# Kernel optimization log

Measured on AMD Instinct MI355X. Metric: run time of the kernel, lower is better.

## Reference

```python
import jax, jax.numpy as jnp
import numpy as np

NEG_SLOPE = 0.2  # PyG GATConv default negative_slope


def _gat_conv(h, src, dst, N, W, a_src, a_dst, b, heads):
    """PyG GATConv (eval mode, self-loops already in src/dst).
    h: [N, F_in], W: [F_in, heads*C], a_src/a_dst: [heads, C], b: [heads*C]."""
    C = W.shape[1] // heads
    hl = (h @ W).reshape(N, heads, C)                      # [N,H,C]
    al_s = jnp.einsum('nhc,hc->nh', hl, a_src)             # [N,H]
    al_d = jnp.einsum('nhc,hc->nh', hl, a_dst)             # [N,H]
    e = jax.nn.leaky_relu(al_s[src] + al_d[dst], NEG_SLOPE)  # [E,H]
    # segment softmax over incoming edges of each destination node
    m = jax.ops.segment_max(e, dst, num_segments=N)        # [N,H]
    ex = jnp.exp(e - m[dst])
    s = jax.ops.segment_sum(ex, dst, num_segments=N)
    alpha = ex / (s[dst] + 1e-16)                          # [E,H]
    out = jax.ops.segment_sum(hl[src] * alpha[:, :, None], dst, num_segments=N)
    return out.reshape(N, heads * C) + b


def setup_inputs() -> dict:
    key = jax.random.key(0)
    ks = jax.random.split(key, 16)
    N, E, D = 30000, 240000, 64
    NUM_ENT, NUM_REL, NUM_DRUGS = 100000, 64, 200
    sc = 0.1
    return {
        'x': jax.random.randint(ks[0], (N,), 0, NUM_ENT),
        'edge_index': jax.random.randint(ks[1], (2, E), 0, N),
        'edge_type': jax.random.randint(ks[2], (N,), 0, NUM_REL),
        'ent_emb': jax.random.normal(ks[3], (NUM_ENT, D), jnp.float32) * sc,
        'rel_emb': jax.random.normal(ks[4], (NUM_REL, D), jnp.float32) * sc,
        'W1': jax.random.normal(ks[5], (2 * D, 8 * D), jnp.float32) * sc,
        'att1_src': jax.random.normal(ks[6], (8, D), jnp.float32) * sc,
        'att1_dst': jax.random.normal(ks[7], (8, D), jnp.float32) * sc,
        'b1': jax.random.normal(ks[8], (8 * D,), jnp.float32) * sc,
        'W2': jax.random.normal(ks[9], (9 * D, D), jnp.float32) * sc,
        'att2_src': jax.random.normal(ks[10], (1, D), jnp.float32) * sc,
        'att2_dst': jax.random.normal(ks[11], (1, D), jnp.float32) * sc,
        'b2': jax.random.normal(ks[12], (D,), jnp.float32) * sc,
        'fc_w': jax.random.normal(ks[13], (D, NUM_DRUGS), jnp.float32) * sc,
        'fc_b': jax.random.normal(ks[14], (NUM_DRUGS,), jnp.float32) * sc,
    }


def reference(x, edge_index, edge_type, ent_emb, rel_emb, W1, att1_src, att1_dst, b1,
              W2, att2_src, att2_dst, b2, fc_w, fc_b):
    N = x.shape[0]
    loop = jnp.arange(N)
    src = jnp.concatenate([edge_index[0], loop])  # GATConv add_self_loops=True
    dst = jnp.concatenate([edge_index[1], loop])
    ent = ent_emb[x]                               # [N,D]
    rel = rel_emb[edge_type]                       # [N,D]
    h = jnp.concatenate([ent, rel], axis=-1)       # [N,2D]  (dropout is identity in eval)
    h = jax.nn.elu(_gat_conv(h, src, dst, N, W1, att1_src, att1_dst, b1, heads=8))  # [N,8D]
    h = jnp.concatenate([h, ent], axis=-1)         # [N,9D]
    h = jax.nn.elu(_gat_conv(h, src, dst, N, W2, att2_src, att2_dst, b2, heads=1))  # [N,D]
    g = jnp.mean(h, axis=0, keepdims=True)         # [1,D]
    return g @ fc_w + fc_b                         # [1,num_drugs]
```

## Files before the change

### kernel.cpp

```cpp
#include <hip/hip_runtime.h>
#include <math.h>

#define NEG_SLOPE 0.2f

typedef __attribute__((ext_vector_type(8))) short short8;
typedef __attribute__((ext_vector_type(4))) float f32x4;
typedef __attribute__((ext_vector_type(2))) float f32x2;

__device__ __forceinline__ float lrelu(float v) { return v > 0.f ? v : NEG_SLOPE * v; }
__device__ __forceinline__ float elu(float v) { return v > 0.f ? v : (__expf(v) - 1.f); }
__device__ __forceinline__ unsigned short f2b(float f) {
    unsigned u = __float_as_uint(f);
    return (unsigned short)((u + 0x7FFFu + ((u >> 16) & 1u)) >> 16);
}
__device__ __forceinline__ float blo(unsigned v) { return __uint_as_float(v << 16); }
__device__ __forceinline__ float bhi(unsigned v) { return __uint_as_float(v & 0xFFFF0000u); }
__device__ __forceinline__ unsigned packb(float a, float b) {
    return ((unsigned)f2b(b) << 16) | (unsigned)f2b(a);
}
__device__ __forceinline__ unsigned short pack8(float a, float b) {
    return (unsigned short)(__builtin_amdgcn_cvt_pk_fp8_f32(a, b, 0, false) & 0xFFFF);
}
__device__ __forceinline__ f32x2 unpack8(unsigned v) {
    return __builtin_amdgcn_cvt_pk_f32_fp8((int)v, false);
}
__device__ __forceinline__ f32x2 unpack8hi(unsigned v) {
    return __builtin_amdgcn_cvt_pk_f32_fp8((int)v, true);
}
__device__ __forceinline__ unsigned bpack_trunc(f32x2 f) {
    return (__float_as_uint(f.y) & 0xFFFF0000u) | (__float_as_uint(f.x) >> 16);
}
__device__ __forceinline__ int sw(int r, int o) { return (o ^ (r & 7)) << 3; }

__global__ __launch_bounds__(256) void init_k(int* __restrict__ zbase, int zwords,
                                              const float* __restrict__ W1,
                                              const float* __restrict__ W2,
                                              const float* __restrict__ a1s,
                                              const float* __restrict__ a1d,
                                              unsigned short* __restrict__ wsb,
                                              unsigned short* __restrict__ W1t,
                                              unsigned short* __restrict__ W2t) {
    int t = blockIdx.x * blockDim.x + threadIdx.x;
    int stride = gridDim.x * blockDim.x;
    for (int i = t; i < zwords; i += stride) zbase[i] = 0;
    for (int i = t; i < 2048; i += stride) {
        int hh = i >> 7, k = i & 127, h = hh & 7;
        const float* aw = (hh < 8) ? a1s : a1d;
        const float* wr = W1 + (size_t)k * 512 + h * 64;
        float s_ = 0.f;
#pragma unroll 16
        for (int c = 0; c < 64; c++) s_ += wr[c] * aw[h * 64 + c];
        wsb[i] = f2b(s_);
    }
    for (int i = t; i < 512 * 128; i += stride) {
        int n = i >> 7, kk = i & 127;
        W1t[i] = f2b(W1[(size_t)kk * 512 + n]);
    }
    for (int i = t; i < 64 * 576; i += stride) {
        int n = i / 576, k = i % 576;
        W2t[i] = f2b(W2[(size_t)k * 64 + n]);
    }
}

__global__ void prep_k(const int* __restrict__ x, const int* __restrict__ et,
                       const int* __restrict__ ei,
                       const float* __restrict__ ent_emb, const float* __restrict__ rel_emb,
                       unsigned* __restrict__ h1b2, unsigned short* __restrict__ h1q,
                       int* __restrict__ deg, int N, int E) {
    int t = blockIdx.x * blockDim.x + threadIdx.x;
    if (t < N * 64) {
        int n = t >> 6, j = t & 63;
        float v0, v1;
        if (j < 32) {
            const float* e = ent_emb + (size_t)x[n] * 64 + 2 * j;
            v0 = e[0]; v1 = e[1];
        } else {
            const float* r = rel_emb + (size_t)et[n] * 64 + 2 * (j - 32);
            v0 = r[0]; v1 = r[1];
        }
        h1b2[t] = packb(v0, v1);
        h1q[t] = pack8(v0, v1);
    }
    if (t < E + N) {
        int dst = t < E ? ei[E + t] : t - E;
        atomicAdd(&deg[dst], 1);
    }
}

__global__ __launch_bounds__(256) void attn1_k(const unsigned short* __restrict__ A,
                                               const unsigned short* __restrict__ Bt,
                                               float* __restrict__ als, float* __restrict__ ald,
                                               int M) {
    __shared__ __align__(16) unsigned short As[128 * 128];
    __shared__ __align__(16) unsigned short Bs[16 * 128];
    int tid = threadIdx.x;
    int m0 = blockIdx.x * 128;
    for (int c = tid; c < 2048; c += 256) {
        int r = c >> 4, o = c & 15;
        int gr = m0 + r;
        uint4 v = make_uint4(0u, 0u, 0u, 0u);
        if (gr < M) v = *(const uint4*)(A + (size_t)gr * 128 + o * 8);
        *(uint4*)(As + r * 128 + sw(r, o)) = v;
    }
    if (tid < 256) {
        int r = tid >> 4, o = tid & 15;
        uint4 v = *(const uint4*)(Bt + (size_t)r * 128 + o * 8);
        *(uint4*)(Bs + r * 128 + sw(r, o)) = v;
    }
    __syncthreads();
    int w = tid >> 6, lane = tid & 63;
    int wr = w * 32;
    int m16 = lane & 15, quad = lane >> 4;
    f32x4 acc[2] = {};
#pragma unroll
    for (int kk = 0; kk < 128; kk += 32) {
        int ob = (kk >> 3) + quad;
        short8 b = *(const short8*)(Bs + m16 * 128 + sw(m16, ob));
#pragma unroll
        for (int i = 0; i < 2; i++) {
            int r = wr + i * 16 + m16;
            short8 a = *(const short8*)(As + r * 128 + sw(r, ob));
            acc[i] = __builtin_amdgcn_mfma_f32_16x16x32_bf16(a, b, acc[i], 0, 0, 0);
        }
    }
#pragma unroll
    for (int i = 0; i < 2; i++)
#pragma unroll
        for (int reg = 0; reg < 4; reg++) {
            int row = m0 + wr + i * 16 + quad * 4 + reg;
            if (row < M) {
                if (m16 < 8) als[row * 8 + m16] = acc[i][reg];
                else         ald[row * 8 + (m16 - 8)] = acc[i][reg];
            }
        }
}

__global__ __launch_bounds__(256) void scan_k(const int* __restrict__ deg,
                                              int* __restrict__ offs,
                                              int* __restrict__ bstate,
                                              int N, int Etot, int NB) {
    __shared__ int s[256];
    __shared__ int sbase;
    int b = blockIdx.x, t = threadIdx.x;
    int i = b * 256 + t;
    int v = (i < N) ? deg[i] : 0;
    s[t] = v;
    __syncthreads();
    for (int off = 1; off < 256; off <<= 1) {
        int tmp = (t >= off) ? s[t - off] : 0;
        __syncthreads();
        s[t] += tmp;
        __syncthreads();
    }
    int total = s[255];
    if (t == 0) {
        if (b == 0) {
            atomicExch(&bstate[0], (total << 2) | 2);
            sbase = 0;
        } else {
            atomicExch(&bstate[b], (total << 2) | 1);
            int run = 0;
            for (int p = b - 1; p >= 0;) {
                int stv;
                do { stv = atomicAdd(&bstate[p], 0); } while ((stv & 3) == 0);
                run += (stv >> 2);
                if ((stv & 3) == 2) break;
                p--;
            }
            atomicExch(&bstate[b], ((run + total) << 2) | 2);
            sbase = run;
        }
    }
    __syncthreads();
    if (i < N) offs[i] = sbase + s[t] - v;
    if (b == NB - 1 && t == 0) offs[N] = Etot;
}

__global__ void fill_k(const int* __restrict__ ei, int E, int N,
                       const int* __restrict__ offs, int* __restrict__ cursor,
                       int* __restrict__ csr) {
    int e = blockIdx.x * blockDim.x + threadIdx.x;
    if (e >= E + N) return;
    int src = e < E ? ei[e] : e - E;
    int dst = e < E ? ei[E + e] : e - E;
    int pos = offs[dst] + atomicAdd(&cursor[dst], 1);
    csr[pos] = src;
}

__global__ __launch_bounds__(256) void aggG_k(const unsigned short* __restrict__ h1q,
                                              const unsigned* __restrict__ h1b2,
                                              const float* __restrict__ als1,
                                              const float* __restrict__ ald1,
                                              const int* __restrict__ offs,
                                              const int* __restrict__ csr,
                                              unsigned short* __restrict__ Gq,
                                              unsigned* __restrict__ h2u, int N) {
    int wv = threadIdx.x >> 6;
    int t = threadIdx.x & 63;
    int n = blockIdx.x * 4 + wv;
    if (n >= N) return;
    int hh = t & 7;
    float dl = ald1[n * 8 + hh];
    int p0 = offs[n], p1 = offs[n + 1];
    float a0[8] = {}, a1[8] = {};
    float ssacc = 0.f;
    int p = p0;
    for (; p + 1 < p1; p += 2) {
        int sA = csr[p], sB = csr[p + 1];
        float lA = als1[sA * 8 + hh];
        float lB = als1[sB * 8 + hh];
        unsigned hA = h1q[(size_t)sA * 64 + t];
        unsigned hB = h1q[(size_t)sB * 64 + t];
        float xA = __expf(lrelu(lA + dl));
        float xB = __expf(lrelu(lB + dl));
        ssacc += xA + xB;
        f32x2 fA = unpack8(hA);
        f32x2 fB = unpack8(hB);
        float evA[8], evB[8];
#pragma unroll
        for (int h = 0; h < 8; h++) { evA[h] = __shfl(xA, h, 64); evB[h] = __shfl(xB, h, 64); }
#pragma unroll
        for (int h = 0; h < 8; h++) {
            a0[h] += evA[h] * fA.x + evB[h] * fB.x;
            a1[h] += evA[h] * fA.y + evB[h] * fB.y;
        }
    }
    if (p < p1) {
        int sA = csr[p];
        float xA = __expf(lrelu(als1[sA * 8 + hh] + dl));
        ssacc += xA;
        f32x2 fA = unpack8(h1q[(size_t)sA * 64 + t]);
        float evA[8];
#pragma unroll
        for (int h = 0; h < 8; h++) evA[h] = __shfl(xA, h, 64);
#pragma unroll
        for (int h = 0; h < 8; h++) { a0[h] += evA[h] * fA.x; a1[h] += evA[h] * fA.y; }
    }
#pragma unroll
    for (int h = 0; h < 8; h++) {
        float iv = 8.f / (__shfl(ssacc, h, 64) + 1e-16f);
        Gq[(size_t)(n * 8 + h) * 64 + t] = pack8(a0[h] * iv, a1[h] * iv);
    }
    if (t < 32)
        h2u[(size_t)n * 288 + 256 + t] = h1b2[(size_t)n * 64 + t];
}

__global__ __launch_bounds__(256) void gemmG_k(const unsigned char* __restrict__ Gq8,
                                               const unsigned short* __restrict__ W1t,
                                               const float* __restrict__ b1,
                                               unsigned short* __restrict__ h2, int M) {
    __shared__ __align__(16) unsigned short As[128 * 128];
    __shared__ __align__(16) unsigned short Bs[64 * 128];
    int tid = threadIdx.x;
    int m0 = blockIdx.x * 128, h = blockIdx.y;
    for (int c = tid; c < 1024; c += 256) {
        int r = c >> 3, o = c & 7;
        int gr = m0 + r;
        uint4 v = make_uint4(0u, 0u, 0u, 0u);
        if (gr < M) v = *(const uint4*)(Gq8 + ((size_t)gr * 8 + h) * 128 + o * 16);
        uint4 w0, w1;
        w0.x = bpack_trunc(unpack8(v.x));   w0.y = bpack_trunc(unpack8hi(v.x));
        w0.z = bpack_trunc(unpack8(v.y));   w0.w = bpack_trunc(unpack8hi(v.y));
        w1.x = bpack_trunc(unpack8(v.z));   w1.y = bpack_trunc(unpack8hi(v.z));
        w1.z = bpack_trunc(unpack8(v.w));   w1.w = bpack_trunc(unpack8hi(v.w));
        *(uint4*)(As + r * 128 + sw(r, 2 * o)) = w0;
        *(uint4*)(As + r * 128 + sw(r, 2 * o + 1)) = w1;
    }
    for (int c = tid; c < 1024; c += 256) {
        int r = c >> 4, o = c & 15;
        uint4 v = *(const uint4*)(W1t + (size_t)(h * 64 + r) * 128 + o * 8);
        *(uint4*)(Bs + r * 128 + sw(r, o)) = v;
    }
    __syncthreads();
    int w = tid >> 6, lane = tid & 63;
    int wr = w * 32;
    int m16 = lane & 15, quad = lane >> 4;
    f32x4 acc[2][4] = {};
#pragma unroll
    for (int kk = 0; kk < 128; kk += 32) {
        int ob = (kk >> 3) + quad;
        short8 b[4];
#pragma unroll
        for (int j = 0; j < 4; j++) {
            int r = j * 16 + m16;
            b[j] = *(const short8*)(Bs + r * 128 + sw(r, ob));
        }
#pragma unroll
        for (int i = 0; i < 2; i++) {
            int r = wr + i * 16 + m16;
            short8 a = *(const short8*)(As + r * 128 + sw(r, ob));
#pragma unroll
            for (int j = 0; j < 4; j++)
                acc[i][j] = __builtin_amdgcn_mfma_f32_16x16x32_bf16(a, b[j], acc[i][j], 0, 0, 0);
        }
    }
#pragma unroll
    for (int i = 0; i < 2; i++)
#pragma unroll
        for (int j = 0; j < 4; j++)
#pragma unroll
            for (int reg = 0; reg < 4; reg++) {
                int row = m0 + wr + i * 16 + quad * 4 + reg;
                int col = h * 64 + j * 16 + m16;
                if (row < M)
                    h2[(size_t)row * 576 + col] = f2b(elu(acc[i][j][reg] * 0.125f + b1[col]));
            }
}

__global__ __launch_bounds__(256) void gemm2_k(const unsigned short* __restrict__ A,
                                               const unsigned short* __restrict__ Bt,
                                               const float* __restrict__ a2s,
                                               const float* __restrict__ a2d,
                                               unsigned char* __restrict__ hl2q,
                                               float* __restrict__ als2,
                                               float* __restrict__ ald2, int M) {
    __shared__ __align__(16) unsigned short As[64 * 64];
    __shared__ __align__(16) unsigned short Bs[64 * 64];
    int tid = threadIdx.x;
    int m0 = blockIdx.x * 64;
    int w = tid >> 6, lane = tid & 63;
    int m16 = lane & 15, quad = lane >> 4;
    f32x4 acc[4] = {};
    for (int k0 = 0; k0 < 576; k0 += 64) {
        __syncthreads();
        for (int c = tid; c < 512; c += 256) {
            int r = c >> 3, o = c & 7;
            int gr = m0 + r;
            uint4 v = make_uint4(0u, 0u, 0u, 0u);
            if (gr < M) v = *(const uint4*)(A + (size_t)gr * 576 + k0 + o * 8);
            *(uint4*)(As + r * 64 + sw(r, o)) = v;
        }
        for (int c = tid; c < 512; c += 256) {
            int r = c >> 3, o = c & 7;
            uint4 v = *(const uint4*)(Bt + (size_t)r * 576 + k0 + o * 8);
            *(uint4*)(Bs + r * 64 + sw(r, o)) = v;
        }
        __syncthreads();
#pragma unroll
        for (int kk = 0; kk < 64; kk += 32) {
            int ob = (kk >> 3) + quad;
            int r = w * 16 + m16;
            short8 a = *(const short8*)(As + r * 64 + sw(r, ob));
#pragma unroll
            for (int j = 0; j < 4; j++) {
                int rb = j * 16 + m16;
                short8 b = *(const short8*)(Bs + rb * 64 + sw(rb, ob));
                acc[j] = __builtin_amdgcn_mfma_f32_16x16x32_bf16(a, b, acc[j], 0, 0, 0);
            }
        }
    }
#pragma unroll
    for (int j = 0; j < 4; j++)
#pragma unroll
        for (int reg = 0; reg < 4; reg++) {
            int row = m0 + w * 16 + quad * 4 + reg;
            int col = j * 16 + m16;
            if (row < M)
                hl2q[(size_t)row * 64 + col] =
                    (unsigned char)(__builtin_amdgcn_cvt_pk_fp8_f32(acc[j][reg], 0.f, 0, false) & 0xFF);
        }
    float sa[4] = {}, sd[4] = {};
#pragma unroll
    for (int j = 0; j < 4; j++) {
        int col = j * 16 + m16;
        float as_ = a2s[col], ad_ = a2d[col];
#pragma unroll
        for (int reg = 0; reg < 4; reg++) {
            sa[reg] += acc[j][reg] * as_;
            sd[reg] += acc[j][reg] * ad_;
        }
    }
#pragma unroll
    for (int m = 1; m < 16; m <<= 1)
#pragma unroll
        for (int reg = 0; reg < 4; reg++) {
            sa[reg] += __shfl_xor(sa[reg], m, 64);
            sd[reg] += __shfl_xor(sd[reg], m, 64);
        }
    if (m16 == 0)
#pragma unroll
        for (int reg = 0; reg < 4; reg++) {
            int row = m0 + w * 16 + quad * 4 + reg;
            if (row < M) { als2[row] = sa[reg]; ald2[row] = sd[reg]; }
        }
}

__global__ __launch_bounds__(256) void agg2_k(const unsigned short* __restrict__ hl2q16,
                                              const float* __restrict__ als2,
                                              const float* __restrict__ ald2,
                                              const float* __restrict__ b2,
                                              const int* __restrict__ offs,
                                              const int* __restrict__ csr,
                                              float* __restrict__ gpart, int N) {
    __shared__ float red[512];
    int slot = threadIdx.x >> 5, l = threadIdx.x & 31;
    int n = blockIdx.x * 8 + slot;
    float v0 = 0.f, v1 = 0.f;
    if (n < N) {
        float dl = ald2[n];
        int p0 = offs[n], p1 = offs[n + 1];
        float a0 = 0.f, a1 = 0.f, ssum = 0.f;
        int p = p0;
        for (; p + 1 < p1; p += 2) {
            int sA = csr[p], sB = csr[p + 1];
            float lA = als2[sA], lB = als2[sB];
            unsigned hA = hl2q16[(size_t)sA * 32 + l];
            unsigned hB = hl2q16[(size_t)sB * 32 + l];
            float xA = __expf(lrelu(lA + dl));
            float xB = __expf(lrelu(lB + dl));
            ssum += xA + xB;
            f32x2 fA = unpack8(hA), fB = unpack8(hB);
            a0 += xA * fA.x + xB * fB.x;
            a1 += xA * fA.y + xB * fB.y;
        }
        if (p < p1) {
            int sA = csr[p];
            float xA = __expf(lrelu(als2[sA] + dl));
            ssum += xA;
            f32x2 fA = unpack8(hl2q16[(size_t)sA * 32 + l]);
            a0 += xA * fA.x;
            a1 += xA * fA.y;
        }
        float inv = 1.f / (ssum + 1e-16f);
        v0 = elu(a0 * inv + b2[2 * l]);
        v1 = elu(a1 * inv + b2[2 * l + 1]);
    }
    red[slot * 64 + 2 * l] = v0;
    red[slot * 64 + 2 * l + 1] = v1;
    __syncthreads();
    if (threadIdx.x < 64) {
        float s = 0.f;
#pragma unroll
        for (int ss = 0; ss < 8; ss++) s += red[ss * 64 + threadIdx.x];
        gpart[(size_t)blockIdx.x * 64 + threadIdx.x] = s;
    }
}

__global__ __launch_bounds__(256) void colredfinal_k(const float* __restrict__ gpart,
                                                     float* __restrict__ gsum,
                                                     int* __restrict__ done,
                                                     const float* __restrict__ fcw,
                                                     const float* __restrict__ fcb,
                                                     float* __restrict__ out,
                                                     int NBL, int N, int NCB) {
    __shared__ float red[256];
    __shared__ int isLast;
    int t = threadIdx.x;
    int c = t & 63, rg = t >> 6;
    int bend = blockIdx.x * 256 + 256; if (bend > NBL) bend = NBL;
    float acc = 0.f;
    for (int b = blockIdx.x * 256 + rg; b < bend; b += 4)
        acc += gpart[(size_t)b * 64 + c];
    red[t] = acc;
    __syncthreads();
    if (t < 64) atomicAdd(&gsum[c], red[c] + red[c + 64] + red[c + 128] + red[c + 192]);
    __threadfence();
    if (t == 0) {
        int old = atomicAdd(done, 1);
        isLast = (old == NCB - 1) ? 1 : 0;
    }
    __syncthreads();
    if (isLast) {
        __shared__ float g[64];
        if (t < 64) g[t] = atomicAdd(&gsum[t], 0.f) / (float)N;
        __syncthreads();
        if (t < 200) {
            float a = fcb[t];
#pragma unroll
            for (int cc = 0; cc < 64; cc++) a += g[cc] * fcw[cc * 200 + t];
            out[t] = a;
        }
    }
}

extern "C" void kernel_launch(void* const* d_in, const int* in_sizes, int n_in,
                              void* d_out, int out_size, void* d_ws, size_t ws_size,
                              hipStream_t stream) {
    const int* x = (const int*)d_in[0];
    const int* ei = (const int*)d_in[1];
    const int* et = (const int*)d_in[2];
    const float* ent_emb = (const float*)d_in[3];
    const float* rel_emb = (const float*)d_in[4];
    const float* W1 = (const float*)d_in[5];
    const float* a1s = (const float*)d_in[6];
    const float* a1d = (const float*)d_in[7];
    const float* b1 = (const float*)d_in[8];
    const float* W2 = (const float*)d_in[9];
    const float* a2s = (const float*)d_in[10];
    const float* a2d = (const float*)d_in[11];
    const float* b2 = (const float*)d_in[12];
    const float* fcw = (const float*)d_in[13];
    const float* fcb = (const float*)d_in[14];
    float* out = (float*)d_out;

    int N = in_sizes[0];
    int E = in_sizes[1] / 2;
    int Etot = E + N;
    int NB = (N + 255) / 256;
    int NBL = (N + 7) / 8;
    int NCB = (NBL + 255) / 256;

    char* p = (char*)d_ws;
    auto alloc = [&](size_t bytes) -> char* {
        char* r = p;
        p += (bytes + 255) & ~(size_t)255;
        return r;
    };
    unsigned* h1b2 = (unsigned*)alloc((size_t)N * 64 * 4);
    unsigned short* h1q = (unsigned short*)alloc((size_t)N * 64 * 2);
    unsigned short* wsb = (unsigned short*)alloc(2048 * 2);
    unsigned short* W1t = (unsigned short*)alloc((size_t)512 * 128 * 2);
    unsigned short* W2t = (unsigned short*)alloc((size_t)64 * 576 * 2);
    float* als1 = (float*)alloc((size_t)N * 8 * 4);
    float* ald1 = (float*)alloc((size_t)N * 8 * 4);
    unsigned short* Gq = (unsigned short*)alloc((size_t)N * 512 * 2);
    unsigned short* h2  = (unsigned short*)alloc((size_t)N * 576 * 2);
    unsigned char* hl2q = (unsigned char*)alloc((size_t)N * 64);
    float* als2 = (float*)alloc((size_t)N * 4);
    float* ald2 = (float*)alloc((size_t)N * 4);
    float* gpart = (float*)alloc((size_t)NBL * 64 * 4);
    int* offs   = (int*)alloc((size_t)(N + 1) * 4);
    int* csr    = (int*)alloc((size_t)Etot * 4);
    char* z0 = p;
    int* deg    = (int*)alloc((size_t)N * 4);
    int* cursor = (int*)alloc((size_t)N * 4);
    float* gsum = (float*)alloc(64 * 4);
    int* done   = (int*)alloc(4);
    int* bstate = (int*)alloc((size_t)NB * 4);
    size_t zwords = (size_t)(p - z0) / 4;

    int tb = 256;
    init_k<<<256, tb, 0, stream>>>((int*)z0, (int)zwords, W1, W2, a1s, a1d, wsb, W1t, W2t);
    prep_k<<<(N * 64 + tb - 1) / tb, tb, 0, stream>>>(x, et, ei, ent_emb, rel_emb,
                                                      h1b2, h1q, deg, N, E);
    attn1_k<<<(N + 127) / 128, 256, 0, stream>>>((const unsigned short*)h1b2, wsb, als1, ald1, N);
    scan_k<<<NB, 256, 0, stream>>>(deg, offs, bstate, N, Etot, NB);
    fill_k<<<(Etot + tb - 1) / tb, tb, 0, stream>>>(ei, E, N, offs, cursor, csr);
    aggG_k<<<(N + 3) / 4, 256, 0, stream>>>(h1q, h1b2, als1, ald1, offs, csr, Gq, (unsigned*)h2, N);
    gemmG_k<<<dim3((N + 127) / 128, 8), 256, 0, stream>>>((const unsigned char*)Gq, W1t, b1, h2, N);
    gemm2_k<<<(N + 63) / 64, 256, 0, stream>>>(h2, W2t, a2s, a2d, hl2q, als2, ald2, N);
    agg2_k<<<NBL, 256, 0, stream>>>((const unsigned short*)hl2q, als2, ald2, b2, offs, csr, gpart, N);
    colredfinal_k<<<NCB, 256, 0, stream>>>(gpart, gsum, done, fcw, fcb, out, NBL, N, NCB);
}
```

Baseline: 270.5 us.

## Precompute layer-1 edge attention weights and softmax sums during CSR fill

New measurement: 368.8 us. 36.4% more time.

```diff
diff --git a/kernel.cpp b/kernel.cpp
--- a/kernel.cpp
+++ b/kernel.cpp
@@ -178,19 +178,41 @@
 
 __global__ void fill_k(const int* __restrict__ ei, int E, int N,
                        const int* __restrict__ offs, int* __restrict__ cursor,
-                       int* __restrict__ csr) {
+                       const float* __restrict__ als1, const float* __restrict__ ald1,
+                       int* __restrict__ csr, float* __restrict__ ex1,
+                       float* __restrict__ ssum) {
     int e = blockIdx.x * blockDim.x + threadIdx.x;
     if (e >= E + N) return;
     int src = e < E ? ei[e] : e - E;
     int dst = e < E ? ei[E + e] : e - E;
     int pos = offs[dst] + atomicAdd(&cursor[dst], 1);
     csr[pos] = src;
+    float4 s0 = *(const float4*)(als1 + src * 8);
+    float4 s1 = *(const float4*)(als1 + src * 8 + 4);
+    float4 d0 = *(const float4*)(ald1 + dst * 8);
+    float4 d1 = *(const float4*)(ald1 + dst * 8 + 4);
+    float4 x0, x1;
+    x0.x = __expf(lrelu(s0.x + d0.x));
+    x0.y = __expf(lrelu(s0.y + d0.y));
+    x0.z = __expf(lrelu(s0.z + d0.z));
+    x0.w = __expf(lrelu(s0.w + d0.w));
+    x1.x = __expf(lrelu(s1.x + d1.x));
+    x1.y = __expf(lrelu(s1.y + d1.y));
+    x1.z = __expf(lrelu(s1.z + d1.z));
+    x1.w = __expf(lrelu(s1.w + d1.w));
+    *(float4*)(ex1 + (size_t)pos * 8) = x0;
+    *(float4*)(ex1 + (size_t)pos * 8 + 4) = x1;
+    float* sb = ssum + dst * 8;
+    atomicAdd(sb + 0, x0.x); atomicAdd(sb + 1, x0.y);
+    atomicAdd(sb + 2, x0.z); atomicAdd(sb + 3, x0.w);
+    atomicAdd(sb + 4, x1.x); atomicAdd(sb + 5, x1.y);
+    atomicAdd(sb + 6, x1.z); atomicAdd(sb + 7, x1.w);
 }
 
 __global__ __launch_bounds__(256) void aggG_k(const unsigned short* __restrict__ h1q,
                                               const unsigned* __restrict__ h1b2,
-                                              const float* __restrict__ als1,
-                                              const float* __restrict__ ald1,
+                                              const float* __restrict__ ex1,
+                                              const float* __restrict__ ssum,
                                               const int* __restrict__ offs,
                                               const int* __restrict__ csr,
                                               unsigned short* __restrict__ Gq,
@@ -199,26 +221,20 @@
     int t = threadIdx.x & 63;
     int n = blockIdx.x * 4 + wv;
     if (n >= N) return;
-    int hh = t & 7;
-    float dl = ald1[n * 8 + hh];
     int p0 = offs[n], p1 = offs[n + 1];
     float a0[8] = {}, a1[8] = {};
-    float ssacc = 0.f;
     int p = p0;
     for (; p + 1 < p1; p += 2) {
         int sA = csr[p], sB = csr[p + 1];
-        float lA = als1[sA * 8 + hh];
-        float lB = als1[sB * 8 + hh];
-        unsigned hA = h1q[(size_t)sA * 64 + t];
-        unsigned hB = h1q[(size_t)sB * 64 + t];
-        float xA = __expf(lrelu(lA + dl));
-        float xB = __expf(lrelu(lB + dl));
-        ssacc += xA + xB;
-        f32x2 fA = unpack8(hA);
-        f32x2 fB = unpack8(hB);
-        float evA[8], evB[8];
-#pragma unroll
-        for (int h = 0; h < 8; h++) { evA[h] = __shfl(xA, h, 64); evB[h] = __shfl(xB, h, 64); }
+        float4 eA0 = *(const float4*)(ex1 + (size_t)p * 8);
+        float4 eA1 = *(const float4*)(ex1 + (size_t)p * 8 + 4);
+        float4 eB0 = *(const float4*)(ex1 + (size_t)p * 8 + 8);
+        float4 eB1 = *(const float4*)(ex1 + (size_t)p * 8 + 12);
+        unsigned hA = h1q[sA * 64 + t];
+        unsigned hB = h1q[sB * 64 + t];
+        f32x2 fA = unpack8(hA), fB = unpack8(hB);
+        float evA[8] = {eA0.x, eA0.y, eA0.z, eA0.w, eA1.x, eA1.y, eA1.z, eA1.w};
+        float evB[8] = {eB0.x, eB0.y, eB0.z, eB0.w, eB1.x, eB1.y, eB1.z, eB1.w};
 #pragma unroll
         for (int h = 0; h < 8; h++) {
             a0[h] += evA[h] * fA.x + evB[h] * fB.x;
@@ -227,22 +243,23 @@
     }
     if (p < p1) {
         int sA = csr[p];
-        float xA = __expf(lrelu(als1[sA * 8 + hh] + dl));
-        ssacc += xA;
-        f32x2 fA = unpack8(h1q[(size_t)sA * 64 + t]);
-        float evA[8];
-#pragma unroll
-        for (int h = 0; h < 8; h++) evA[h] = __shfl(xA, h, 64);
+        float4 eA0 = *(const float4*)(ex1 + (size_t)p * 8);
+        float4 eA1 = *(const float4*)(ex1 + (size_t)p * 8 + 4);
+        f32x2 fA = unpack8(h1q[sA * 64 + t]);
+        float evA[8] = {eA0.x, eA0.y, eA0.z, eA0.w, eA1.x, eA1.y, eA1.z, eA1.w};
 #pragma unroll
         for (int h = 0; h < 8; h++) { a0[h] += evA[h] * fA.x; a1[h] += evA[h] * fA.y; }
     }
+    float4 s0 = *(const float4*)(ssum + n * 8);
+    float4 s1 = *(const float4*)(ssum + n * 8 + 4);
+    float sv[8] = {s0.x, s0.y, s0.z, s0.w, s1.x, s1.y, s1.z, s1.w};
 #pragma unroll
     for (int h = 0; h < 8; h++) {
-        float iv = 8.f / (__shfl(ssacc, h, 64) + 1e-16f);
-        Gq[(size_t)(n * 8 + h) * 64 + t] = pack8(a0[h] * iv, a1[h] * iv);
+        float iv = 8.f / (sv[h] + 1e-16f);
+        Gq[(n * 8 + h) * 64 + t] = pack8(a0[h] * iv, a1[h] * iv);
     }
     if (t < 32)
-        h2u[(size_t)n * 288 + 256 + t] = h1b2[(size_t)n * 64 + t];
+        h2u[(size_t)n * 288 + 256 + t] = h1b2[n * 64 + t];
 }
 
 __global__ __launch_bounds__(256) void gemmG_k(const unsigned char* __restrict__ Gq8,
@@ -404,8 +421,8 @@
         for (; p + 1 < p1; p += 2) {
             int sA = csr[p], sB = csr[p + 1];
             float lA = als2[sA], lB = als2[sB];
-            unsigned hA = hl2q16[(size_t)sA * 32 + l];
-            unsigned hB = hl2q16[(size_t)sB * 32 + l];
+            unsigned hA = hl2q16[sA * 32 + l];
+            unsigned hB = hl2q16[sB * 32 + l];
             float xA = __expf(lrelu(lA + dl));
             float xB = __expf(lrelu(lB + dl));
             ssum += xA + xB;
@@ -417,7 +434,7 @@
             int sA = csr[p];
             float xA = __expf(lrelu(als2[sA] + dl));
             ssum += xA;
-            f32x2 fA = unpack8(hl2q16[(size_t)sA * 32 + l]);
+            f32x2 fA = unpack8(hl2q16[sA * 32 + l]);
             a0 += xA * fA.x;
             a1 += xA * fA.y;
         }
@@ -513,6 +530,7 @@
     unsigned short* W2t = (unsigned short*)alloc((size_t)64 * 576 * 2);
     float* als1 = (float*)alloc((size_t)N * 8 * 4);
     float* ald1 = (float*)alloc((size_t)N * 8 * 4);
+    float* ex1  = (float*)alloc((size_t)Etot * 8 * 4);
     unsigned short* Gq = (unsigned short*)alloc((size_t)N * 512 * 2);
     unsigned short* h2  = (unsigned short*)alloc((size_t)N * 576 * 2);
     unsigned char* hl2q = (unsigned char*)alloc((size_t)N * 64);
@@ -527,6 +545,7 @@
     float* gsum = (float*)alloc(64 * 4);
     int* done   = (int*)alloc(4);
     int* bstate = (int*)alloc((size_t)NB * 4);
+    float* ssum = (float*)alloc((size_t)N * 8 * 4);
     size_t zwords = (size_t)(p - z0) / 4;
 
     int tb = 256;
@@ -535,8 +554,9 @@
                                                       h1b2, h1q, deg, N, E);
     attn1_k<<<(N + 127) / 128, 256, 0, stream>>>((const unsigned short*)h1b2, wsb, als1, ald1, N);
     scan_k<<<NB, 256, 0, stream>>>(deg, offs, bstate, N, Etot, NB);
-    fill_k<<<(Etot + tb - 1) / tb, tb, 0, stream>>>(ei, E, N, offs, cursor, csr);
-    aggG_k<<<(N + 3) / 4, 256, 0, stream>>>(h1q, h1b2, als1, ald1, offs, csr, Gq, (unsigned*)h2, N);
+    fill_k<<<(Etot + tb - 1) / tb, tb, 0, stream>>>(ei, E, N, offs, cursor, als1, ald1,
+                                                    csr, ex1, ssum);
+    aggG_k<<<(N + 3) / 4, 256, 0, stream>>>(h1q, h1b2, ex1, ssum, offs, csr, Gq, (unsigned*)h2, N);
     gemmG_k<<<dim3((N + 127) / 128, 8), 256, 0, stream>>>((const unsigned char*)Gq, W1t, b1, h2, N);
     gemm2_k<<<(N + 63) / 64, 256, 0, stream>>>(h2, W2t, a2s, a2d, hl2q, als2, ald2, N);
     agg2_k<<<NBL, 256, 0, stream>>>((const unsigned short*)hl2q, als2, ald2, b2, offs, csr, gpart, N);
```
